# Performance work log

Hardware: AMD Instinct MI355X
Metric: run time of the kernel (lower is better)

The kernel has to match this reference:

```python
import jax, jax.numpy as jnp
import numpy as np

B, N, C, H = 2, 2048, 768, 12
HD = C // H  # head dim = 64


def setup_inputs() -> dict:
    key = jax.random.key(0)
    k1, k2, k3 = jax.random.split(key, 3)
    x = jax.random.normal(k1, (B, N, C), dtype=jnp.float32)
    w_qkv = jax.random.normal(k2, (C, 3 * C), dtype=jnp.float32) * (C ** -0.5)
    w_proj = jax.random.normal(k3, (C, C), dtype=jnp.float32) * (C ** -0.5)
    b_proj = jnp.zeros((C,), dtype=jnp.float32)
    return {"x": x, "w_qkv": w_qkv, "w_proj": w_proj, "b_proj": b_proj}


def reference(x, w_qkv, w_proj, b_proj):
    scale = HD ** -0.5
    # qkv projection: [B,N,3C] -> [3,B,H,N,HD]
    qkv = (x @ w_qkv).reshape(B, N, 3, H, HD).transpose(2, 0, 3, 1, 4)
    q, k, v = qkv[0], qkv[1], qkv[2]
    # explicit QK^T softmax V (materializes [B,H,N,N] scores, as in source)
    attn = jnp.einsum("bhqd,bhkd->bhqk", q, k) * scale
    attn = jax.nn.softmax(attn, axis=-1)
    out = jnp.einsum("bhqk,bhkd->bhqd", attn, v)
    out = out.transpose(0, 2, 1, 3).reshape(B, N, C)
    return out @ w_proj + b_proj
```

## Files before the change

kernel.cpp:

```cpp
#include <hip/hip_runtime.h>

#define C_DIM 768
#define NSEQ 2048
#define H_DIM 12
#define HD 64
#define M_ROWS 4096

typedef float f32x4 __attribute__((ext_vector_type(4)));
typedef short bf16x8 __attribute__((ext_vector_type(8)));
typedef _Float16 f16x8 __attribute__((ext_vector_type(8)));
typedef _Float16 f16x4 __attribute__((ext_vector_type(4)));
typedef __fp16 fp16x2 __attribute__((ext_vector_type(2)));
typedef unsigned short u16;

#define MFMA_PV(a, b, c) __builtin_amdgcn_mfma_f32_16x16x16f16(a, b, c, 0, 0, 0)

__device__ __forceinline__ u16 f2bf(float f) {
  union { float f; unsigned u; } v; v.f = f;
  unsigned u = v.u + 0x7FFFu + ((v.u >> 16) & 1u);
  return (u16)(u >> 16);
}

__global__ __launch_bounds__(256) void cvt_x_kernel(const float* __restrict__ in,
                                                    u16* __restrict__ out, int n4) {
  int i = blockIdx.x * 256 + threadIdx.x;
  if (i < n4) {
    float4 v = ((const float4*)in)[i];
    ushort4 o;
    o.x = f2bf(v.x); o.y = f2bf(v.y); o.z = f2bf(v.z); o.w = f2bf(v.w);
    ((ushort4*)out)[i] = o;
  }
}

__global__ __launch_bounds__(256) void transpose_cvt_kernel(const float* __restrict__ in,
                                                            u16* __restrict__ out,
                                                            int R, int Cc) {
  __shared__ float t[32][33];
  int tx = threadIdx.x & 31, ty = threadIdx.x >> 5;
  int c0 = blockIdx.x * 32, r0 = blockIdx.y * 32;
#pragma unroll
  for (int i = 0; i < 4; i++)
    t[ty + i * 8][tx] = in[(size_t)(r0 + ty + i * 8) * Cc + c0 + tx];
  __syncthreads();
#pragma unroll
  for (int i = 0; i < 4; i++)
    out[(size_t)(c0 + ty + i * 8) * R + r0 + tx] = f2bf(t[tx][ty + i * 8]);
}

__device__ __forceinline__ void gemm_core_128(const u16* __restrict__ A,
                                              const u16* __restrict__ BT,
                                              int m0, int n0,
                                              u16* la, u16* lb, f32x4 acc[4][4]) {
  const int K = C_DIM;
  int tid = threadIdx.x;
  int lane = tid & 63, wave = tid >> 6;
  int wm = (wave >> 1) * 64, wn = (wave & 1) * 64;
  int quad = lane >> 4, l16 = lane & 15;

  int rowA = tid >> 2, cj = tid & 3;
  const u16* pa0 = A + (size_t)(m0 + rowA) * K + cj * 8;
  const u16* pa1 = pa0 + (size_t)64 * K;
  const u16* pb0 = BT + (size_t)(n0 + rowA) * K + cj * 8;
  const u16* pb1 = pb0 + (size_t)64 * K;
  int swz = ((cj ^ (rowA & 3)) * 8);
  int wr0 = rowA * 32 + swz;
  int wr1 = (rowA + 64) * 32 + swz;

  for (int k0 = 0; k0 < K; k0 += 32) {
    uint4 va0 = *(const uint4*)(pa0 + k0);
    uint4 va1 = *(const uint4*)(pa1 + k0);
    uint4 vb0 = *(const uint4*)(pb0 + k0);
    uint4 vb1 = *(const uint4*)(pb1 + k0);
    __syncthreads();
    *(uint4*)(la + wr0) = va0;
    *(uint4*)(la + wr1) = va1;
    *(uint4*)(lb + wr0) = vb0;
    *(uint4*)(lb + wr1) = vb1;
    __syncthreads();
    bf16x8 af[4], bfr[4];
#pragma unroll
    for (int mt = 0; mt < 4; mt++) {
      int r = wm + mt * 16 + l16;
      af[mt] = *(const bf16x8*)(la + r * 32 + ((quad ^ (r & 3)) * 8));
    }
#pragma unroll
    for (int nt = 0; nt < 4; nt++) {
      int r = wn + nt * 16 + l16;
      bfr[nt] = *(const bf16x8*)(lb + r * 32 + ((quad ^ (r & 3)) * 8));
    }
#pragma unroll
    for (int mt = 0; mt < 4; mt++)
#pragma unroll
      for (int nt = 0; nt < 4; nt++)
        acc[mt][nt] = __builtin_amdgcn_mfma_f32_16x16x32_bf16(af[mt], bfr[nt], acc[mt][nt], 0, 0, 0);
  }
}

#define Q_PRESCALE 0.18033688011112042f
__global__ __launch_bounds__(256) void gemm_qkv_kernel(const u16* __restrict__ A,
                                                       const u16* __restrict__ BT,
                                                       _Float16* __restrict__ qb,
                                                       _Float16* __restrict__ kb,
                                                       _Float16* __restrict__ vtb) {
  __shared__ __align__(16) u16 la[128 * 32];
  __shared__ __align__(16) u16 lb[128 * 32];
  f32x4 acc[4][4] = {};
  int m0 = blockIdx.x * 128, n0 = blockIdx.y * 128;
  gemm_core_128(A, BT, m0, n0, la, lb, acc);

  int lane = threadIdx.x & 63, wave = threadIdx.x >> 6;
  int wm = (wave >> 1) * 64, wn = (wave & 1) * 64;
  int quad = lane >> 4, l16 = lane & 15;
#pragma unroll
  for (int mt = 0; mt < 4; mt++) {
#pragma unroll
    for (int nt = 0; nt < 4; nt++) {
      int gn = n0 + wn + nt * 16 + l16;
      int which = gn / C_DIM;
      int cc = gn - which * C_DIM;
      int h = cc >> 6, d = cc & 63;
      int gm0 = m0 + wm + mt * 16 + quad * 4;
      int b = gm0 >> 11, n = gm0 & 2047;
      size_t bh = (size_t)(b * H_DIM + h);
      if (which == 2) {
        f16x4 hv;
#pragma unroll
        for (int r = 0; r < 4; r++) hv[r] = (_Float16)acc[mt][nt][r];
        *(f16x4*)(vtb + (bh * HD + d) * NSEQ + n) = hv;
      } else if (which == 0) {
#pragma unroll
        for (int r = 0; r < 4; r++)
          qb[(bh * NSEQ + n + r) * HD + d] = (_Float16)(acc[mt][nt][r] * Q_PRESCALE);
      } else {
#pragma unroll
        for (int r = 0; r < 4; r++)
          kb[(bh * NSEQ + n + r) * HD + d] = (_Float16)acc[mt][nt][r];
      }
    }
  }
}

__global__ __launch_bounds__(256) void gemm_proj_kernel(const u16* __restrict__ A,
                                                        const u16* __restrict__ BT,
                                                        const float* __restrict__ bias,
                                                        float* __restrict__ out) {
  __shared__ __align__(16) u16 la[128 * 32];
  __shared__ __align__(16) u16 lb[128 * 32];
  f32x4 acc[4][4] = {};
  int m0 = blockIdx.x * 128, n0 = blockIdx.y * 128;
  gemm_core_128(A, BT, m0, n0, la, lb, acc);

  int lane = threadIdx.x & 63, wave = threadIdx.x >> 6;
  int wm = (wave >> 1) * 64, wn = (wave & 1) * 64;
  int quad = lane >> 4, l16 = lane & 15;
#pragma unroll
  for (int mt = 0; mt < 4; mt++) {
#pragma unroll
    for (int nt = 0; nt < 4; nt++) {
      int gn = n0 + wn + nt * 16 + l16;
      float bv = bias[gn];
#pragma unroll
      for (int r = 0; r < 4; r++) {
        int gm = m0 + wm + mt * 16 + quad * 4 + r;
        out[(size_t)gm * C_DIM + gn] = acc[mt][nt][r] + bv;
      }
    }
  }
}

__global__ __launch_bounds__(256) void attn_kernel(const _Float16* __restrict__ qb,
                                                   const _Float16* __restrict__ kb,
                                                   const _Float16* __restrict__ vtb,
                                                   u16* __restrict__ attn) {
  __shared__ __align__(16) u16 lk[2][64 * 72];
  __shared__ __align__(16) u16 lv[2][64 * 72];
  int bh = blockIdx.y, qblk = blockIdx.x;
  int tid = threadIdx.x, lane = tid & 63, wave = tid >> 6;
  int quad = lane >> 4, l16 = lane & 15;

  const _Float16* q_bh = qb + (size_t)bh * NSEQ * HD;
  const u16* k_bh = (const u16*)(kb + (size_t)bh * NSEQ * HD);
  const u16* v_bh = (const u16*)(vtb + (size_t)bh * HD * NSEQ);

  int q0 = qblk * 128 + wave * 32 + l16;
  f16x8 qf[2][2];
#pragma unroll
  for (int qt = 0; qt < 2; qt++) {
    const _Float16* qp = q_bh + (size_t)(q0 + qt * 16) * HD + quad * 8;
    qf[qt][0] = *(const f16x8*)qp;
    qf[qt][1] = *(const f16x8*)(qp + 32);
  }

  f32x4 o[2][4] = {};
  float l_i[2] = {0.f, 0.f};

  int srow = tid >> 3, scj = tid & 7;
  const u16* kp0 = k_bh + (size_t)srow * HD + scj * 8;
  const u16* kp1 = kp0 + (size_t)32 * HD;
  const u16* vp0 = v_bh + (size_t)srow * NSEQ + scj * 8;
  const u16* vp1 = vp0 + (size_t)32 * NSEQ;
  int w0 = srow * 72 + scj * 8, w1 = (srow + 32) * 72 + scj * 8;

  {
    *(uint4*)(lk[0] + w0) = *(const uint4*)(kp0);
    *(uint4*)(lk[0] + w1) = *(const uint4*)(kp1);
    *(uint4*)(lv[0] + w0) = *(const uint4*)(vp0);
    *(uint4*)(lv[0] + w1) = *(const uint4*)(vp1);
  }

  for (int kt = 0; kt < 32; kt++) {
    int cur = kt & 1, nxt = cur ^ 1;
    __syncthreads();

    uint4 rk0, rk1, rv0, rv1;
    if (kt < 31) {
      int k0 = (kt + 1) * 64;
      rk0 = *(const uint4*)(kp0 + (size_t)k0 * HD);
      rk1 = *(const uint4*)(kp1 + (size_t)k0 * HD);
      rv0 = *(const uint4*)(vp0 + k0);
      rv1 = *(const uint4*)(vp1 + k0);
    }

    f32x4 s0[4], s1[4];
#pragma unroll
    for (int nt = 0; nt < 4; nt++) {
      const u16* kp = lk[cur] + (nt * 16 + l16) * 72 + quad * 8;
      f16x8 kf0 = *(const f16x8*)kp;
      f16x8 kf1 = *(const f16x8*)(kp + 32);
      f32x4 t0 = {}, t1 = {};
      t0 = __builtin_amdgcn_mfma_f32_16x16x32_f16(kf0, qf[0][0], t0, 0, 0, 0);
      t0 = __builtin_amdgcn_mfma_f32_16x16x32_f16(kf1, qf[0][1], t0, 0, 0, 0);
      t1 = __builtin_amdgcn_mfma_f32_16x16x32_f16(kf0, qf[1][0], t1, 0, 0, 0);
      t1 = __builtin_amdgcn_mfma_f32_16x16x32_f16(kf1, qf[1][1], t1, 0, 0, 0);
      s0[nt] = t0; s1[nt] = t1;
    }

#pragma unroll
    for (int nt = 0; nt < 4; nt++) {
      float a0 = __builtin_amdgcn_exp2f(s0[nt][0]);
      float a1 = __builtin_amdgcn_exp2f(s0[nt][1]);
      float a2 = __builtin_amdgcn_exp2f(s0[nt][2]);
      float a3 = __builtin_amdgcn_exp2f(s0[nt][3]);
      l_i[0] += (a0 + a1) + (a2 + a3);
      float b0 = __builtin_amdgcn_exp2f(s1[nt][0]);
      float b1 = __builtin_amdgcn_exp2f(s1[nt][1]);
      float b2 = __builtin_amdgcn_exp2f(s1[nt][2]);
      float b3 = __builtin_amdgcn_exp2f(s1[nt][3]);
      l_i[1] += (b0 + b1) + (b2 + b3);
      union { fp16x2 h2[2]; f16x4 h4; } pa, pb;
      pa.h2[0] = __builtin_amdgcn_cvt_pkrtz(a0, a1);
      pa.h2[1] = __builtin_amdgcn_cvt_pkrtz(a2, a3);
      pb.h2[0] = __builtin_amdgcn_cvt_pkrtz(b0, b1);
      pb.h2[1] = __builtin_amdgcn_cvt_pkrtz(b2, b3);
#pragma unroll
      for (int dt = 0; dt < 4; dt++) {
        f16x4 vf = *(const f16x4*)(lv[cur] + (dt * 16 + l16) * 72 + nt * 16 + quad * 4);
        o[0][dt] = MFMA_PV(vf, pa.h4, o[0][dt]);
        o[1][dt] = MFMA_PV(vf, pb.h4, o[1][dt]);
      }
    }

    if (kt < 31) {
      *(uint4*)(lk[nxt] + w0) = rk0;
      *(uint4*)(lk[nxt] + w1) = rk1;
      *(uint4*)(lv[nxt] + w0) = rv0;
      *(uint4*)(lv[nxt] + w1) = rv1;
    }
  }

#pragma unroll
  for (int qt = 0; qt < 2; qt++) {
    l_i[qt] += __shfl_xor(l_i[qt], 16);
    l_i[qt] += __shfl_xor(l_i[qt], 32);
  }

  int b = bh / H_DIM, h = bh % H_DIM;
#pragma unroll
  for (int qt = 0; qt < 2; qt++) {
    float inv = 1.f / l_i[qt];
    int q = q0 + qt * 16;
    u16* orow = attn + (size_t)(b * NSEQ + q) * C_DIM + h * HD;
#pragma unroll
    for (int dt = 0; dt < 4; dt++) {
      ushort4 ov;
      ov.x = f2bf(o[qt][dt][0] * inv);
      ov.y = f2bf(o[qt][dt][1] * inv);
      ov.z = f2bf(o[qt][dt][2] * inv);
      ov.w = f2bf(o[qt][dt][3] * inv);
      *(ushort4*)(orow + dt * 16 + quad * 4) = ov;
    }
  }
}

extern "C" void kernel_launch(void* const* d_in, const int* in_sizes, int n_in,
                              void* d_out, int out_size, void* d_ws, size_t ws_size,
                              hipStream_t stream) {
  const float* x = (const float*)d_in[0];
  const float* w_qkv = (const float*)d_in[1];
  const float* w_proj = (const float*)d_in[2];
  const float* b_proj = (const float*)d_in[3];
  float* out = (float*)d_out;

  char* ws = (char*)d_ws;
  u16* x_bf        = (u16*)(ws);
  u16* wqkvT       = (u16*)(ws + 6291456);
  u16* wprojT      = (u16*)(ws + 9830400);
  _Float16* qb     = (_Float16*)(ws + 11010048);
  _Float16* kb     = (_Float16*)(ws + 17301504);
  _Float16* vtb    = (_Float16*)(ws + 23592960);
  u16* attn        = x_bf;

  cvt_x_kernel<<<3072, 256, 0, stream>>>(x, x_bf, M_ROWS * C_DIM / 4);
  transpose_cvt_kernel<<<dim3(72, 24), 256, 0, stream>>>(w_qkv, wqkvT, C_DIM, 3 * C_DIM);
  transpose_cvt_kernel<<<dim3(24, 24), 256, 0, stream>>>(w_proj, wprojT, C_DIM, C_DIM);
  gemm_qkv_kernel<<<dim3(32, 18), 256, 0, stream>>>(x_bf, wqkvT, qb, kb, vtb);
  attn_kernel<<<dim3(16, 24), 256, 0, stream>>>(qb, kb, vtb, attn);
  gemm_proj_kernel<<<dim3(32, 6), 256, 0, stream>>>(attn, wprojT, b_proj, out);
}
```

Baseline: 180.1 us.

## Use direct global-to-LDS loads, smaller attention blocks, finer proj tiles, fused transposes

Replaces register-staged global loads with global_load_lds DMA into XOR-swizzled shared memory in both GEMM cores and the attention K/V staging. The attention kernel drops to 128 threads and 64 queries per block, doubling the grid. The projection GEMM switches to 64-row tiles for more blocks. The two weight-transpose launches are merged into one. The aim is to cut VGPR staging and register pressure, add occupancy and cut launch overhead. The price is new swizzle indexing and less per-block reuse of each K/V tile.

```diff
diff --git a/kernel.cpp b/kernel.cpp
--- a/kernel.cpp
+++ b/kernel.cpp
@@ -14,6 +14,12 @@
 typedef unsigned short u16;
 
 #define MFMA_PV(a, b, c) __builtin_amdgcn_mfma_f32_16x16x16f16(a, b, c, 0, 0, 0)
+
+typedef unsigned int __attribute__((address_space(1))) as1_uint;
+typedef unsigned int __attribute__((address_space(3))) as3_uint;
+__device__ __forceinline__ void dma16(const void* g, void* l) {
+  __builtin_amdgcn_global_load_lds((const as1_uint*)g, (as3_uint*)l, 16, 0, 0);
+}
 
 __device__ __forceinline__ u16 f2bf(float f) {
   union { float f; unsigned u; } v; v.f = f;
@@ -32,9 +38,14 @@
   }
 }
 
-__global__ __launch_bounds__(256) void transpose_cvt_kernel(const float* __restrict__ in,
-                                                            u16* __restrict__ out,
-                                                            int R, int Cc) {
+__global__ __launch_bounds__(256) void transpose_cvt_kernel(const float* __restrict__ wq,
+                                                            const float* __restrict__ wp,
+                                                            u16* __restrict__ outq,
+                                                            u16* __restrict__ outp) {
+  const float* in; u16* out; int Cc;
+  if (blockIdx.z == 0) { in = wq; out = outq; Cc = 3 * C_DIM; }
+  else { if (blockIdx.x >= 24) return; in = wp; out = outp; Cc = C_DIM; }
+  const int R = C_DIM;
   __shared__ float t[32][33];
   int tx = threadIdx.x & 31, ty = threadIdx.x >> 5;
   int c0 = blockIdx.x * 32, r0 = blockIdx.y * 32;
@@ -52,30 +63,27 @@
                                               int m0, int n0,
                                               u16* la, u16* lb, f32x4 acc[4][4]) {
   const int K = C_DIM;
-  int tid = threadIdx.x;
-  int lane = tid & 63, wave = tid >> 6;
+  int tid = threadIdx.x, lane = tid & 63, wave = tid >> 6;
   int wm = (wave >> 1) * 64, wn = (wave & 1) * 64;
   int quad = lane >> 4, l16 = lane & 15;
 
-  int rowA = tid >> 2, cj = tid & 3;
-  const u16* pa0 = A + (size_t)(m0 + rowA) * K + cj * 8;
-  const u16* pa1 = pa0 + (size_t)64 * K;
-  const u16* pb0 = BT + (size_t)(n0 + rowA) * K + cj * 8;
-  const u16* pb1 = pb0 + (size_t)64 * K;
-  int swz = ((cj ^ (rowA & 3)) * 8);
-  int wr0 = rowA * 32 + swz;
-  int wr1 = (rowA + 64) * 32 + swz;
+  int r0 = wave * 16 + (lane >> 2);
+  int sw = (((lane & 3) ^ (r0 & 3)) * 8);
+  const u16* ga0 = A + (size_t)(m0 + r0) * K + sw;
+  const u16* ga1 = A + (size_t)(m0 + r0 + 64) * K + sw;
+  const u16* gb0 = BT + (size_t)(n0 + r0) * K + sw;
+  const u16* gb1 = BT + (size_t)(n0 + r0 + 64) * K + sw;
+  u16* lA0 = la + wave * 16 * 32;
+  u16* lA1 = lA0 + 64 * 32;
+  u16* lB0 = lb + wave * 16 * 32;
+  u16* lB1 = lB0 + 64 * 32;
 
   for (int k0 = 0; k0 < K; k0 += 32) {
-    uint4 va0 = *(const uint4*)(pa0 + k0);
-    uint4 va1 = *(const uint4*)(pa1 + k0);
-    uint4 vb0 = *(const uint4*)(pb0 + k0);
-    uint4 vb1 = *(const uint4*)(pb1 + k0);
-    __syncthreads();
-    *(uint4*)(la + wr0) = va0;
-    *(uint4*)(la + wr1) = va1;
-    *(uint4*)(lb + wr0) = vb0;
-    *(uint4*)(lb + wr1) = vb1;
+    __syncthreads();
+    dma16(ga0 + k0, lA0);
+    dma16(ga1 + k0, lA1);
+    dma16(gb0 + k0, lB0);
+    dma16(gb1 + k0, lB1);
     __syncthreads();
     bf16x8 af[4], bfr[4];
 #pragma unroll
@@ -90,6 +98,49 @@
     }
 #pragma unroll
     for (int mt = 0; mt < 4; mt++)
+#pragma unroll
+      for (int nt = 0; nt < 4; nt++)
+        acc[mt][nt] = __builtin_amdgcn_mfma_f32_16x16x32_bf16(af[mt], bfr[nt], acc[mt][nt], 0, 0, 0);
+  }
+}
+
+__device__ __forceinline__ void gemm_core_64(const u16* __restrict__ A,
+                                             const u16* __restrict__ BT,
+                                             int m0, int n0,
+                                             u16* la, u16* lb, f32x4 acc[2][4]) {
+  const int K = C_DIM;
+  int tid = threadIdx.x, lane = tid & 63, wave = tid >> 6;
+  int wm = (wave >> 1) * 32, wn = (wave & 1) * 64;
+  int quad = lane >> 4, l16 = lane & 15;
+
+  int r0 = wave * 16 + (lane >> 2);
+  int sw = (((lane & 3) ^ (r0 & 3)) * 8);
+  const u16* ga0 = A + (size_t)(m0 + r0) * K + sw;
+  const u16* gb0 = BT + (size_t)(n0 + r0) * K + sw;
+  const u16* gb1 = BT + (size_t)(n0 + r0 + 64) * K + sw;
+  u16* lA0 = la + wave * 16 * 32;
+  u16* lB0 = lb + wave * 16 * 32;
+  u16* lB1 = lB0 + 64 * 32;
+
+  for (int k0 = 0; k0 < K; k0 += 32) {
+    __syncthreads();
+    dma16(ga0 + k0, lA0);
+    dma16(gb0 + k0, lB0);
+    dma16(gb1 + k0, lB1);
+    __syncthreads();
+    bf16x8 af[2], bfr[4];
+#pragma unroll
+    for (int mt = 0; mt < 2; mt++) {
+      int r = wm + mt * 16 + l16;
+      af[mt] = *(const bf16x8*)(la + r * 32 + ((quad ^ (r & 3)) * 8));
+    }
+#pragma unroll
+    for (int nt = 0; nt < 4; nt++) {
+      int r = wn + nt * 16 + l16;
+      bfr[nt] = *(const bf16x8*)(lb + r * 32 + ((quad ^ (r & 3)) * 8));
+    }
+#pragma unroll
+    for (int mt = 0; mt < 2; mt++)
 #pragma unroll
       for (int nt = 0; nt < 4; nt++)
         acc[mt][nt] = __builtin_amdgcn_mfma_f32_16x16x32_bf16(af[mt], bfr[nt], acc[mt][nt], 0, 0, 0);
@@ -144,17 +195,17 @@
                                                         const u16* __restrict__ BT,
                                                         const float* __restrict__ bias,
                                                         float* __restrict__ out) {
-  __shared__ __align__(16) u16 la[128 * 32];
+  __shared__ __align__(16) u16 la[64 * 32];
   __shared__ __align__(16) u16 lb[128 * 32];
-  f32x4 acc[4][4] = {};
-  int m0 = blockIdx.x * 128, n0 = blockIdx.y * 128;
-  gemm_core_128(A, BT, m0, n0, la, lb, acc);
+  f32x4 acc[2][4] = {};
+  int m0 = blockIdx.x * 64, n0 = blockIdx.y * 128;
+  gemm_core_64(A, BT, m0, n0, la, lb, acc);
 
   int lane = threadIdx.x & 63, wave = threadIdx.x >> 6;
-  int wm = (wave >> 1) * 64, wn = (wave & 1) * 64;
-  int quad = lane >> 4, l16 = lane & 15;
-#pragma unroll
-  for (int mt = 0; mt < 4; mt++) {
+  int wm = (wave >> 1) * 32, wn = (wave & 1) * 64;
+  int quad = lane >> 4, l16 = lane & 15;
+#pragma unroll
+  for (int mt = 0; mt < 2; mt++) {
 #pragma unroll
     for (int nt = 0; nt < 4; nt++) {
       int gn = n0 + wn + nt * 16 + l16;
@@ -168,12 +219,12 @@
   }
 }
 
-__global__ __launch_bounds__(256) void attn_kernel(const _Float16* __restrict__ qb,
+__global__ __launch_bounds__(128) void attn_kernel(const _Float16* __restrict__ qb,
                                                    const _Float16* __restrict__ kb,
                                                    const _Float16* __restrict__ vtb,
                                                    u16* __restrict__ attn) {
-  __shared__ __align__(16) u16 lk[2][64 * 72];
-  __shared__ __align__(16) u16 lv[2][64 * 72];
+  __shared__ __align__(16) u16 lk[2][64 * 64];
+  __shared__ __align__(16) u16 lv[2][64 * 64];
   int bh = blockIdx.y, qblk = blockIdx.x;
   int tid = threadIdx.x, lane = tid & 63, wave = tid >> 6;
   int quad = lane >> 4, l16 = lane & 15;
@@ -182,7 +233,7 @@
   const u16* k_bh = (const u16*)(kb + (size_t)bh * NSEQ * HD);
   const u16* v_bh = (const u16*)(vtb + (size_t)bh * HD * NSEQ);
 
-  int q0 = qblk * 128 + wave * 32 + l16;
+  int q0 = qblk * 64 + wave * 32 + l16;
   f16x8 qf[2][2];
 #pragma unroll
   for (int qt = 0; qt < 2; qt++) {
@@ -194,39 +245,34 @@
   f32x4 o[2][4] = {};
   float l_i[2] = {0.f, 0.f};
 
-  int srow = tid >> 3, scj = tid & 7;
-  const u16* kp0 = k_bh + (size_t)srow * HD + scj * 8;
-  const u16* kp1 = kp0 + (size_t)32 * HD;
-  const u16* vp0 = v_bh + (size_t)srow * NSEQ + scj * 8;
-  const u16* vp1 = vp0 + (size_t)32 * NSEQ;
-  int w0 = srow * 72 + scj * 8, w1 = (srow + 32) * 72 + scj * 8;
-
-  {
-    *(uint4*)(lk[0] + w0) = *(const uint4*)(kp0);
-    *(uint4*)(lk[0] + w1) = *(const uint4*)(kp1);
-    *(uint4*)(lv[0] + w0) = *(const uint4*)(vp0);
-    *(uint4*)(lv[0] + w1) = *(const uint4*)(vp1);
-  }
+  int sr = wave * 32 + (lane >> 3);
+  int sw = (((lane & 7) ^ (sr & 7)) * 8);
+  const u16* gk = k_bh + (size_t)sr * HD + sw;
+  const u16* gv = v_bh + (size_t)sr * NSEQ + sw;
+  int lbase = wave * 32 * 64;
+
+#define STAGE_KV(buf, kk)                                            \
+  {                                                                  \
+    _Pragma("unroll") for (int j = 0; j < 4; j++) {                  \
+      dma16(gk + (size_t)((kk) + j * 8) * HD, &lk[buf][lbase + j * 512]); \
+      dma16(gv + (size_t)(j * 8) * NSEQ + (kk), &lv[buf][lbase + j * 512]); \
+    }                                                                \
+  }
+
+  STAGE_KV(0, 0);
 
   for (int kt = 0; kt < 32; kt++) {
-    int cur = kt & 1, nxt = cur ^ 1;
-    __syncthreads();
-
-    uint4 rk0, rk1, rv0, rv1;
-    if (kt < 31) {
-      int k0 = (kt + 1) * 64;
-      rk0 = *(const uint4*)(kp0 + (size_t)k0 * HD);
-      rk1 = *(const uint4*)(kp1 + (size_t)k0 * HD);
-      rv0 = *(const uint4*)(vp0 + k0);
-      rv1 = *(const uint4*)(vp1 + k0);
-    }
+    int cur = kt & 1;
+    __syncthreads();
+    if (kt < 31) STAGE_KV(cur ^ 1, (kt + 1) * 64);
 
     f32x4 s0[4], s1[4];
 #pragma unroll
     for (int nt = 0; nt < 4; nt++) {
-      const u16* kp = lk[cur] + (nt * 16 + l16) * 72 + quad * 8;
-      f16x8 kf0 = *(const f16x8*)kp;
-      f16x8 kf1 = *(const f16x8*)(kp + 32);
+      const u16* kbp = lk[cur] + (nt * 16 + l16) * 64;
+      int rs = l16 & 7;
+      f16x8 kf0 = *(const f16x8*)(kbp + ((quad ^ rs) * 8));
+      f16x8 kf1 = *(const f16x8*)(kbp + (((quad + 4) ^ rs) * 8));
       f32x4 t0 = {}, t1 = {};
       t0 = __builtin_amdgcn_mfma_f32_16x16x32_f16(kf0, qf[0][0], t0, 0, 0, 0);
       t0 = __builtin_amdgcn_mfma_f32_16x16x32_f16(kf1, qf[0][1], t0, 0, 0, 0);
@@ -254,17 +300,12 @@
       pb.h2[1] = __builtin_amdgcn_cvt_pkrtz(b2, b3);
 #pragma unroll
       for (int dt = 0; dt < 4; dt++) {
-        f16x4 vf = *(const f16x4*)(lv[cur] + (dt * 16 + l16) * 72 + nt * 16 + quad * 4);
+        int r = dt * 16 + l16;
+        int c = nt * 2 + (quad >> 1);
+        f16x4 vf = *(const f16x4*)(lv[cur] + r * 64 + ((c ^ (l16 & 7)) * 8) + (quad & 1) * 4);
         o[0][dt] = MFMA_PV(vf, pa.h4, o[0][dt]);
         o[1][dt] = MFMA_PV(vf, pb.h4, o[1][dt]);
       }
-    }
-
-    if (kt < 31) {
-      *(uint4*)(lk[nxt] + w0) = rk0;
-      *(uint4*)(lk[nxt] + w1) = rk1;
-      *(uint4*)(lv[nxt] + w0) = rv0;
-      *(uint4*)(lv[nxt] + w1) = rv1;
     }
   }
 
@@ -311,9 +352,8 @@
   u16* attn        = x_bf;
 
   cvt_x_kernel<<<3072, 256, 0, stream>>>(x, x_bf, M_ROWS * C_DIM / 4);
-  transpose_cvt_kernel<<<dim3(72, 24), 256, 0, stream>>>(w_qkv, wqkvT, C_DIM, 3 * C_DIM);
-  transpose_cvt_kernel<<<dim3(24, 24), 256, 0, stream>>>(w_proj, wprojT, C_DIM, C_DIM);
+  transpose_cvt_kernel<<<dim3(72, 24, 2), 256, 0, stream>>>(w_qkv, w_proj, wqkvT, wprojT);
   gemm_qkv_kernel<<<dim3(32, 18), 256, 0, stream>>>(x_bf, wqkvT, qb, kb, vtb);
-  attn_kernel<<<dim3(16, 24), 256, 0, stream>>>(qb, kb, vtb, attn);
-  gemm_proj_kernel<<<dim3(32, 6), 256, 0, stream>>>(attn, wprojT, b_proj, out);
-}
+  attn_kernel<<<dim3(32, 24), 128, 0, stream>>>(qb, kb, vtb, attn);
+  gemm_proj_kernel<<<dim3(64, 6), 256, 0, stream>>>(attn, wprojT, b_proj, out);
+}
```

Measured after the change: 174.2 us. -3.3%, faster.
